# Optimization experiments

Measured on AMD Instinct MI355X. Metric: run time of the kernel, lower is better.

Reference implementation:

```python
import jax, jax.numpy as jnp
import numpy as np

EPS = 1e-5

def _bn(x, g, b, m, v):
    # eval-mode BatchNorm over channel dim (x: [N, C])
    return (x - m) * jax.lax.rsqrt(v + EPS) * g + b

def setup_inputs() -> dict:
    key = jax.random.key(0)
    ks = jax.random.split(key, 12)
    B, T, C, H, W = 16, 8, 512, 28, 28
    c8 = C // 8
    inp = {}
    inp['x'] = jax.random.normal(ks[0], (B * T, C, H, W), jnp.float32)
    inp['w1'] = jax.random.normal(ks[1], (c8, C), jnp.float32) * 0.05
    inp['bn1_g'] = jnp.ones((c8,), jnp.float32)
    inp['bn1_b'] = jnp.zeros((c8,), jnp.float32)
    inp['bn1_m'] = jax.random.normal(ks[2], (c8,), jnp.float32) * 0.1
    inp['bn1_v'] = jax.random.uniform(ks[3], (c8,), jnp.float32) + 0.5
    inp['w2'] = jax.random.normal(ks[4], (c8, C), jnp.float32) * 0.05
    inp['bn2_g'] = jnp.ones((c8,), jnp.float32)
    inp['bn2_b'] = jnp.zeros((c8,), jnp.float32)
    inp['bn2_m'] = jax.random.normal(ks[5], (c8,), jnp.float32) * 0.1
    inp['bn2_v'] = jax.random.uniform(ks[6], (c8,), jnp.float32) + 0.5
    inp['Wa_w'] = jax.random.normal(ks[7], (C, c8), jnp.float32) * 0.05
    inp['Wa_b'] = jnp.zeros((C,), jnp.float32)
    inp['gamma_w'] = jax.random.normal(ks[8], (2 * c8,), jnp.float32) * 0.05
    inp['gamma_b'] = jnp.zeros((1,), jnp.float32)
    inp['n_segment'] = T
    return inp

def reference(x, w1, bn1_g, bn1_b, bn1_m, bn1_v, w2, bn2_g, bn2_b, bn2_m, bn2_v, Wa_w, Wa_b, gamma_w, gamma_b, n_segment):
    nt, c, h, w = x.shape
    T = n_segment
    B = nt // T
    # adaptive_avg_pool2d to 1x1 == spatial mean -> [nt, c]
    xv = jnp.mean(x, axis=(2, 3))
    # 1x1 conv on 1x1 spatial map == channel matmul; conv -> BN -> ReLU
    left = jax.nn.relu(_bn(xv @ w1.T, bn1_g, bn1_b, bn1_m, bn1_v)).reshape(B, T, -1)
    right = jax.nn.relu(_bn(xv @ w2.T, bn2_g, bn2_b, bn2_m, bn2_v)).reshape(B, T, -1)
    # temporal difference, pad last step with constant 1 (matches F.pad value=1)
    diff = jnp.concatenate(
        [left[:, :-1] - right[:, 1:], jnp.ones((B, 1, left.shape[-1]), x.dtype)], axis=1)

    def step(g_state, d_t):
        # g_state, d_t: [B, c//8]
        cat = jnp.concatenate([d_t, g_state], axis=1)            # [B, c//4]
        g = jax.nn.sigmoid(cat @ gamma_w + gamma_b[0])[:, None]  # [B, 1] gate
        new = d_t * g + g_state * (1.0 - g)
        att = jax.nn.sigmoid(new @ Wa_w.T + Wa_b)                # [B, c]
        return new, att

    # initial x_global = x_vec_diff[:, -1] (the padded ones slice)
    _, atts = jax.lax.scan(step, diff[:, -1], jnp.swapaxes(diff, 0, 1))
    sig = jnp.swapaxes(atts, 0, 1)                               # [B, T, c]
    out = x.reshape(B, T, c, h, w) * sig[:, :, :, None, None]
    return out.reshape(nt, c, h, w)
```

## Files before the change

kernel.cpp:

```cpp
#include <hip/hip_runtime.h>
#include <hip/hip_bf16.h>
#include <math.h>

constexpr int NT  = 128;
constexpr int C   = 512;
constexpr int HW  = 784;
constexpr int C8  = 64;
constexpr int TT  = 8;
constexpr int BB  = 16;
constexpr float EPS = 1e-5f;

__global__ void k_mean(const float* __restrict__ x, float* __restrict__ xv) {
    const int wave = threadIdx.x >> 6;
    const int lane = threadIdx.x & 63;
    const size_t row = (size_t)blockIdx.x * 4 + wave;
    const float4* p = (const float4*)(x + row * HW);
    float s = 0.f;
    #pragma unroll
    for (int j = lane; j < HW / 4; j += 64) {
        float4 v = p[j];
        s += v.x + v.y + v.z + v.w;
    }
    #pragma unroll
    for (int off = 32; off; off >>= 1) s += __shfl_xor(s, off);
    if (lane == 0) xv[row] = s * (1.0f / HW);
}

__global__ void k_lr(const float* __restrict__ xv,
                     const float* __restrict__ w1,
                     const float* __restrict__ g1, const float* __restrict__ b1,
                     const float* __restrict__ m1, const float* __restrict__ v1,
                     const float* __restrict__ w2,
                     const float* __restrict__ g2, const float* __restrict__ b2,
                     const float* __restrict__ m2, const float* __restrict__ v2,
                     float* __restrict__ lr) {
    __shared__ float sx[C];
    const int bt = blockIdx.x;
    for (int i = threadIdx.x; i < C; i += 256) sx[i] = xv[bt * C + i];
    __syncthreads();

    const int out  = threadIdx.x >> 1;
    const int half = threadIdx.x & 1;
    const int j    = out & 63;
    const float* w = (out < C8) ? (w1 + (size_t)j * C) : (w2 + (size_t)j * C);
    const int k0 = half * (C / 2);
    float acc = 0.f;
    #pragma unroll 8
    for (int k = 0; k < C / 2; ++k) acc = fmaf(sx[k0 + k], w[k0 + k], acc);
    acc += __shfl_xor(acc, 1);
    if (half == 0) {
        float y;
        if (out < C8) y = (acc - m1[j]) * rsqrtf(v1[j] + EPS) * g1[j] + b1[j];
        else          y = (acc - m2[j]) * rsqrtf(v2[j] + EPS) * g2[j] + b2[j];
        lr[bt * 2 * C8 + out] = fmaxf(y, 0.f);
    }
}

__global__ void k_scan(const float* __restrict__ lr,
                       const float* __restrict__ gamma_w,
                       const float* __restrict__ gamma_b,
                       float* __restrict__ Nw) {
    const int b = blockIdx.x;
    const int j = threadIdx.x;
    const float gw0 = gamma_w[j];
    const float gw1 = gamma_w[C8 + j];
    const float gb  = gamma_b[0];

    float d[TT];
    #pragma unroll
    for (int t = 0; t < TT - 1; ++t)
        d[t] = lr[(b * TT + t) * (2 * C8) + j]
             - lr[(b * TT + t + 1) * (2 * C8) + C8 + j];
    d[TT - 1] = 1.0f;

    float state = 1.0f;
    #pragma unroll
    for (int t = 0; t < TT; ++t) {
        float part = d[t] * gw0 + state * gw1;
        #pragma unroll
        for (int off = 32; off; off >>= 1) part += __shfl_xor(part, off);
        const float g = 1.f / (1.f + expf(-(part + gb)));
        state = d[t] * g + state * (1.f - g);
        Nw[(b * TT + t) * C8 + j] = state;
    }
}

__global__ void k_att(const float* __restrict__ Nw,
                      const float* __restrict__ Wa_w,
                      const float* __restrict__ Wa_b,
                      float* __restrict__ sig) {
    __shared__ float sn[C8];
    const int bt = blockIdx.x;
    if (threadIdx.x < C8) sn[threadIdx.x] = Nw[bt * C8 + threadIdx.x];
    __syncthreads();
    for (int c = threadIdx.x; c < C; c += 256) {
        const float* w = Wa_w + (size_t)c * C8;
        float acc = Wa_b[c];
        #pragma unroll 16
        for (int k = 0; k < C8; ++k) acc = fmaf(sn[k], w[k], acc);
        sig[bt * C + c] = 1.f / (1.f + expf(-acc));
    }
}

__global__ void k_scale(const float* __restrict__ x,
                        const float* __restrict__ sig,
                        float* __restrict__ out) {
    const int wave = threadIdx.x >> 6;
    const int lane = threadIdx.x & 63;
    const size_t row = (size_t)blockIdx.x * 4 + wave;
    const float s = sig[row];
    const float4* px = (const float4*)(x + row * HW);
    float4*       po = (float4*)(out + row * HW);
    #pragma unroll
    for (int j = lane; j < HW / 4; j += 64) {
        float4 v = px[j];
        v.x *= s; v.y *= s; v.z *= s; v.w *= s;
        po[j] = v;
    }
}

extern "C" void kernel_launch(void* const* d_in, const int* in_sizes, int n_in,
                              void* d_out, int out_size, void* d_ws, size_t ws_size,
                              hipStream_t stream) {
    const float* x     = (const float*)d_in[0];
    const float* w1    = (const float*)d_in[1];
    const float* bn1_g = (const float*)d_in[2];
    const float* bn1_b = (const float*)d_in[3];
    const float* bn1_m = (const float*)d_in[4];
    const float* bn1_v = (const float*)d_in[5];
    const float* w2    = (const float*)d_in[6];
    const float* bn2_g = (const float*)d_in[7];
    const float* bn2_b = (const float*)d_in[8];
    const float* bn2_m = (const float*)d_in[9];
    const float* bn2_v = (const float*)d_in[10];
    const float* Wa_w  = (const float*)d_in[11];
    const float* Wa_b  = (const float*)d_in[12];
    const float* gamma_w = (const float*)d_in[13];
    const float* gamma_b = (const float*)d_in[14];
    float* out = (float*)d_out;

    float* ws  = (float*)d_ws;
    float* xv  = ws;
    float* lr  = xv + NT * C;
    float* Nw  = lr + NT * 2 * C8;
    float* sig = Nw + NT * C8;

    const int rows = NT * C;
    k_mean <<<rows / 4, 256, 0, stream>>>(x, xv);
    k_lr   <<<NT, 256, 0, stream>>>(xv, w1, bn1_g, bn1_b, bn1_m, bn1_v,
                                        w2, bn2_g, bn2_b, bn2_m, bn2_v, lr);
    k_scan <<<BB, 64, 0, stream>>>(lr, gamma_w, gamma_b, Nw);
    k_att  <<<NT, 256, 0, stream>>>(Nw, Wa_w, Wa_b, sig);
    k_scale<<<rows / 4, 256, 0, stream>>>(x, sig, out);
}
```

Baseline: 423.5 us.

## Fuse small middle kernels into one per-batch kernel and widen streaming kernels

Merges the left/right projection, temporal gate scan and attention projection into a single kernel with one block per batch, keeping intermediates in shared memory, which removes two launches and the global round trips between them. The mean and scale kernels now have each wave handle four rows, using four independent loads per iteration and vector sig reads. The scale kernel also writes its output with nontemporal stores. The fused middle kernel runs on only 16 blocks, so its serial matmul work is less parallel than before.

Measured after the change: 453.0 us. 1.07x slower.

```diff
diff --git a/kernel.cpp b/kernel.cpp
--- a/kernel.cpp
+++ b/kernel.cpp
@@ -1,5 +1,4 @@
 #include <hip/hip_runtime.h>
-#include <hip/hip_bf16.h>
 #include <math.h>
 
 constexpr int NT  = 128;
@@ -10,146 +9,184 @@
 constexpr int BB  = 16;
 constexpr float EPS = 1e-5f;
 
-__global__ void k_mean(const float* __restrict__ x, float* __restrict__ xv) {
+typedef float v4f __attribute__((ext_vector_type(4)));
+
+__global__ __launch_bounds__(256) void k_mean(const float* __restrict__ x,
+                                              float* __restrict__ xv) {
     const int wave = threadIdx.x >> 6;
     const int lane = threadIdx.x & 63;
-    const size_t row = (size_t)blockIdx.x * 4 + wave;
-    const float4* p = (const float4*)(x + row * HW);
-    float s = 0.f;
-    #pragma unroll
+    const size_t wid = (size_t)blockIdx.x * 4 + wave;
+    const float4* p = (const float4*)(x + wid * (size_t)(4 * HW));
+    float s0 = 0.f, s1 = 0.f, s2 = 0.f, s3 = 0.f;
     for (int j = lane; j < HW / 4; j += 64) {
-        float4 v = p[j];
-        s += v.x + v.y + v.z + v.w;
+        float4 a = p[j];
+        float4 b = p[j + 196];
+        float4 c = p[j + 392];
+        float4 d = p[j + 588];
+        s0 += (a.x + a.y) + (a.z + a.w);
+        s1 += (b.x + b.y) + (b.z + b.w);
+        s2 += (c.x + c.y) + (c.z + c.w);
+        s3 += (d.x + d.y) + (d.z + d.w);
     }
     #pragma unroll
-    for (int off = 32; off; off >>= 1) s += __shfl_xor(s, off);
-    if (lane == 0) xv[row] = s * (1.0f / HW);
-}
-
-__global__ void k_lr(const float* __restrict__ xv,
-                     const float* __restrict__ w1,
-                     const float* __restrict__ g1, const float* __restrict__ b1,
-                     const float* __restrict__ m1, const float* __restrict__ v1,
-                     const float* __restrict__ w2,
-                     const float* __restrict__ g2, const float* __restrict__ b2,
-                     const float* __restrict__ m2, const float* __restrict__ v2,
-                     float* __restrict__ lr) {
-    __shared__ float sx[C];
-    const int bt = blockIdx.x;
-    for (int i = threadIdx.x; i < C; i += 256) sx[i] = xv[bt * C + i];
-    __syncthreads();
-
-    const int out  = threadIdx.x >> 1;
-    const int half = threadIdx.x & 1;
-    const int j    = out & 63;
-    const float* w = (out < C8) ? (w1 + (size_t)j * C) : (w2 + (size_t)j * C);
-    const int k0 = half * (C / 2);
-    float acc = 0.f;
-    #pragma unroll 8
-    for (int k = 0; k < C / 2; ++k) acc = fmaf(sx[k0 + k], w[k0 + k], acc);
-    acc += __shfl_xor(acc, 1);
-    if (half == 0) {
-        float y;
-        if (out < C8) y = (acc - m1[j]) * rsqrtf(v1[j] + EPS) * g1[j] + b1[j];
-        else          y = (acc - m2[j]) * rsqrtf(v2[j] + EPS) * g2[j] + b2[j];
-        lr[bt * 2 * C8 + out] = fmaxf(y, 0.f);
+    for (int off = 32; off; off >>= 1) {
+        s0 += __shfl_xor(s0, off);
+        s1 += __shfl_xor(s1, off);
+        s2 += __shfl_xor(s2, off);
+        s3 += __shfl_xor(s3, off);
+    }
+    if (lane == 0) {
+        const float inv = 1.0f / HW;
+        ((float4*)xv)[wid] = make_float4(s0 * inv, s1 * inv, s2 * inv, s3 * inv);
     }
 }
 
-__global__ void k_scan(const float* __restrict__ lr,
-                       const float* __restrict__ gamma_w,
-                       const float* __restrict__ gamma_b,
-                       float* __restrict__ Nw) {
+__global__ __launch_bounds__(256) void k_mid(
+        const float* __restrict__ xv,
+        const float* __restrict__ w1,
+        const float* __restrict__ g1, const float* __restrict__ b1,
+        const float* __restrict__ m1, const float* __restrict__ v1,
+        const float* __restrict__ w2,
+        const float* __restrict__ g2, const float* __restrict__ b2,
+        const float* __restrict__ m2, const float* __restrict__ v2,
+        const float* __restrict__ gamma_w, const float* __restrict__ gamma_b,
+        const float* __restrict__ Wa_w, const float* __restrict__ Wa_b,
+        float* __restrict__ sig) {
+    __shared__ float sx[TT * C];
+    __shared__ float slr[TT][2 * C8];
+    __shared__ float sN[TT][C8];
     const int b = blockIdx.x;
-    const int j = threadIdx.x;
-    const float gw0 = gamma_w[j];
-    const float gw1 = gamma_w[C8 + j];
-    const float gb  = gamma_b[0];
 
-    float d[TT];
-    #pragma unroll
-    for (int t = 0; t < TT - 1; ++t)
-        d[t] = lr[(b * TT + t) * (2 * C8) + j]
-             - lr[(b * TT + t + 1) * (2 * C8) + C8 + j];
-    d[TT - 1] = 1.0f;
+    for (int i = threadIdx.x; i < TT * C; i += 256)
+        sx[i] = xv[b * TT * C + i];
+    __syncthreads();
 
-    float state = 1.0f;
-    #pragma unroll
-    for (int t = 0; t < TT; ++t) {
-        float part = d[t] * gw0 + state * gw1;
+    {
+        const int u  = threadIdx.x & 127;
+        const int t0 = threadIdx.x >> 7;
+        const int j  = u & 63;
+        const float* __restrict__ w =
+            (u < C8) ? (w1 + (size_t)j * C) : (w2 + (size_t)j * C);
+        const float* x0 = sx + (t0 + 0) * C;
+        const float* x1 = sx + (t0 + 2) * C;
+        const float* x2 = sx + (t0 + 4) * C;
+        const float* x3 = sx + (t0 + 6) * C;
+        float a0 = 0.f, a1 = 0.f, a2 = 0.f, a3 = 0.f;
+        #pragma unroll 8
+        for (int k = 0; k < C; ++k) {
+            const float wk = w[k];
+            a0 = fmaf(x0[k], wk, a0);
+            a1 = fmaf(x1[k], wk, a1);
+            a2 = fmaf(x2[k], wk, a2);
+            a3 = fmaf(x3[k], wk, a3);
+        }
+        float mm, sc, bb;
+        if (u < C8) { mm = m1[j]; sc = rsqrtf(v1[j] + EPS) * g1[j]; bb = b1[j]; }
+        else        { mm = m2[j]; sc = rsqrtf(v2[j] + EPS) * g2[j]; bb = b2[j]; }
+        slr[t0 + 0][u] = fmaxf(fmaf(a0 - mm, sc, bb), 0.f);
+        slr[t0 + 2][u] = fmaxf(fmaf(a1 - mm, sc, bb), 0.f);
+        slr[t0 + 4][u] = fmaxf(fmaf(a2 - mm, sc, bb), 0.f);
+        slr[t0 + 6][u] = fmaxf(fmaf(a3 - mm, sc, bb), 0.f);
+    }
+    __syncthreads();
+
+    if (threadIdx.x < 64) {
+        const int j = threadIdx.x;
+        const float gw0 = gamma_w[j];
+        const float gw1 = gamma_w[C8 + j];
+        const float gb  = gamma_b[0];
+        float d[TT];
         #pragma unroll
-        for (int off = 32; off; off >>= 1) part += __shfl_xor(part, off);
-        const float g = 1.f / (1.f + expf(-(part + gb)));
-        state = d[t] * g + state * (1.f - g);
-        Nw[(b * TT + t) * C8 + j] = state;
+        for (int t = 0; t < TT - 1; ++t) d[t] = slr[t][j] - slr[t + 1][C8 + j];
+        d[TT - 1] = 1.0f;
+        float state = 1.0f;
+        #pragma unroll
+        for (int t = 0; t < TT; ++t) {
+            float part = d[t] * gw0 + state * gw1;
+            #pragma unroll
+            for (int off = 32; off; off >>= 1) part += __shfl_xor(part, off);
+            const float g = 1.f / (1.f + expf(-(part + gb)));
+            state = d[t] * g + state * (1.f - g);
+            sN[t][j] = state;
+        }
+    }
+    __syncthreads();
+
+    {
+        const int c0 = threadIdx.x;
+        const int c1 = threadIdx.x + 256;
+        const float* __restrict__ wA = Wa_w + (size_t)c0 * C8;
+        const float* __restrict__ wB = Wa_w + (size_t)c1 * C8;
+        const float baseA = Wa_b[c0];
+        const float baseB = Wa_b[c1];
+        for (int t = 0; t < TT; ++t) {
+            const float* n = sN[t];
+            float accA = baseA, accB = baseB;
+            #pragma unroll 8
+            for (int k = 0; k < C8; ++k) {
+                const float nk = n[k];
+                accA = fmaf(nk, wA[k], accA);
+                accB = fmaf(nk, wB[k], accB);
+            }
+            sig[(b * TT + t) * C + c0] = 1.f / (1.f + expf(-accA));
+            sig[(b * TT + t) * C + c1] = 1.f / (1.f + expf(-accB));
+        }
     }
 }
 
-__global__ void k_att(const float* __restrict__ Nw,
-                      const float* __restrict__ Wa_w,
-                      const float* __restrict__ Wa_b,
-                      float* __restrict__ sig) {
-    __shared__ float sn[C8];
-    const int bt = blockIdx.x;
-    if (threadIdx.x < C8) sn[threadIdx.x] = Nw[bt * C8 + threadIdx.x];
-    __syncthreads();
-    for (int c = threadIdx.x; c < C; c += 256) {
-        const float* w = Wa_w + (size_t)c * C8;
-        float acc = Wa_b[c];
-        #pragma unroll 16
-        for (int k = 0; k < C8; ++k) acc = fmaf(sn[k], w[k], acc);
-        sig[bt * C + c] = 1.f / (1.f + expf(-acc));
-    }
-}
-
-__global__ void k_scale(const float* __restrict__ x,
-                        const float* __restrict__ sig,
-                        float* __restrict__ out) {
+__global__ __launch_bounds__(256) void k_scale(const float* __restrict__ x,
+                                               const float* __restrict__ sig,
+                                               float* __restrict__ out) {
     const int wave = threadIdx.x >> 6;
     const int lane = threadIdx.x & 63;
-    const size_t row = (size_t)blockIdx.x * 4 + wave;
-    const float s = sig[row];
-    const float4* px = (const float4*)(x + row * HW);
-    float4*       po = (float4*)(out + row * HW);
-    #pragma unroll
+    const size_t wid = (size_t)blockIdx.x * 4 + wave;
+    const float4 sv = ((const float4*)sig)[wid];
+    const v4f* px = (const v4f*)(x + wid * (size_t)(4 * HW));
+    v4f*       po = (v4f*)(out + wid * (size_t)(4 * HW));
     for (int j = lane; j < HW / 4; j += 64) {
-        float4 v = px[j];
-        v.x *= s; v.y *= s; v.z *= s; v.w *= s;
-        po[j] = v;
+        v4f a = px[j];
+        v4f b = px[j + 196];
+        v4f c = px[j + 392];
+        v4f d = px[j + 588];
+        a = a * sv.x;
+        b = b * sv.y;
+        c = c * sv.z;
+        d = d * sv.w;
+        __builtin_nontemporal_store(a, po + j);
+        __builtin_nontemporal_store(b, po + j + 196);
+        __builtin_nontemporal_store(c, po + j + 392);
+        __builtin_nontemporal_store(d, po + j + 588);
     }
 }
 
 extern "C" void kernel_launch(void* const* d_in, const int* in_sizes, int n_in,
                               void* d_out, int out_size, void* d_ws, size_t ws_size,
                               hipStream_t stream) {
-    const float* x     = (const float*)d_in[0];
-    const float* w1    = (const float*)d_in[1];
-    const float* bn1_g = (const float*)d_in[2];
-    const float* bn1_b = (const float*)d_in[3];
-    const float* bn1_m = (const float*)d_in[4];
-    const float* bn1_v = (const float*)d_in[5];
-    const float* w2    = (const float*)d_in[6];
-    const float* bn2_g = (const float*)d_in[7];
-    const float* bn2_b = (const float*)d_in[8];
-    const float* bn2_m = (const float*)d_in[9];
-    const float* bn2_v = (const float*)d_in[10];
-    const float* Wa_w  = (const float*)d_in[11];
-    const float* Wa_b  = (const float*)d_in[12];
+    const float* x       = (const float*)d_in[0];
+    const float* w1      = (const float*)d_in[1];
+    const float* bn1_g   = (const float*)d_in[2];
+    const float* bn1_b   = (const float*)d_in[3];
+    const float* bn1_m   = (const float*)d_in[4];
+    const float* bn1_v   = (const float*)d_in[5];
+    const float* w2      = (const float*)d_in[6];
+    const float* bn2_g   = (const float*)d_in[7];
+    const float* bn2_b   = (const float*)d_in[8];
+    const float* bn2_m   = (const float*)d_in[9];
+    const float* bn2_v   = (const float*)d_in[10];
+    const float* Wa_w    = (const float*)d_in[11];
+    const float* Wa_b    = (const float*)d_in[12];
     const float* gamma_w = (const float*)d_in[13];
     const float* gamma_b = (const float*)d_in[14];
     float* out = (float*)d_out;
 
     float* ws  = (float*)d_ws;
     float* xv  = ws;
-    float* lr  = xv + NT * C;
-    float* Nw  = lr + NT * 2 * C8;
-    float* sig = Nw + NT * C8;
+    float* sig = xv + NT * C;
 
     const int rows = NT * C;
-    k_mean <<<rows / 4, 256, 0, stream>>>(x, xv);
-    k_lr   <<<NT, 256, 0, stream>>>(xv, w1, bn1_g, bn1_b, bn1_m, bn1_v,
-                                        w2, bn2_g, bn2_b, bn2_m, bn2_v, lr);
-    k_scan <<<BB, 64, 0, stream>>>(lr, gamma_w, gamma_b, Nw);
-    k_att  <<<NT, 256, 0, stream>>>(Nw, Wa_w, Wa_b, sig);
-    k_scale<<<rows / 4, 256, 0, stream>>>(x, sig, out);
+    k_mean <<<rows / 16, 256, 0, stream>>>(x, xv);
+    k_mid  <<<BB, 256, 0, stream>>>(xv, w1, bn1_g, bn1_b, bn1_m, bn1_v,
+                                        w2, bn2_g, bn2_b, bn2_m, bn2_v,
+                                        gamma_w, gamma_b, Wa_w, Wa_b, sig);
+    k_scale<<<rows / 16, 256, 0, stream>>>(x, sig, out);
 }
```
